# Kernel tuning notes

Measured on AMD Instinct MI355X. Metric: run time of the kernel, lower is better.

## Reference

```python
import jax, jax.numpy as jnp
import numpy as np
from jax import lax

B, T, IN, H, OUT = 64, 2048, 128, 256, 1


def setup_inputs() -> dict:
    key = jax.random.key(0)
    ks = jax.random.split(key, 11)
    s_in = 1.0 / np.sqrt(H)
    return {
        "x": jax.random.normal(ks[0], (B, T, IN), dtype=jnp.float32),
        "W_ih0": jax.random.normal(ks[1], (H, IN), dtype=jnp.float32) * s_in,
        "W_hh0": jax.random.normal(ks[2], (H, H), dtype=jnp.float32) * s_in,
        "b_ih0": jax.random.normal(ks[3], (H,), dtype=jnp.float32) * s_in,
        "b_hh0": jax.random.normal(ks[4], (H,), dtype=jnp.float32) * s_in,
        "W_ih1": jax.random.normal(ks[5], (H, H), dtype=jnp.float32) * s_in,
        "W_hh1": jax.random.normal(ks[6], (H, H), dtype=jnp.float32) * s_in,
        "b_ih1": jax.random.normal(ks[7], (H,), dtype=jnp.float32) * s_in,
        "b_hh1": jax.random.normal(ks[8], (H,), dtype=jnp.float32) * s_in,
        "W_fc": jax.random.normal(ks[9], (OUT, H), dtype=jnp.float32) * s_in,
        "b_fc": jax.random.normal(ks[10], (OUT,), dtype=jnp.float32) * s_in,
    }


def _rnn_layer(inp, W_ih, W_hh, b_ih, b_hh):
    # Precompute input projection for all timesteps in one big GEMM: [B,T,H]
    xp = jnp.einsum('bti,hi->bth', inp, W_ih) + b_ih + b_hh
    h0 = jnp.zeros((inp.shape[0], W_hh.shape[0]), dtype=inp.dtype)

    def step(h, xt):  # xt: [B,H]
        h_new = jnp.tanh(xt + h @ W_hh.T)
        return h_new, h_new

    _, hs = lax.scan(step, h0, jnp.swapaxes(xp, 0, 1))  # hs: [T,B,H]
    return jnp.swapaxes(hs, 0, 1)  # [B,T,H]


def reference(x, W_ih0, W_hh0, b_ih0, b_hh0, W_ih1, W_hh1, b_ih1, b_hh1, W_fc, b_fc):
    h1 = _rnn_layer(x, W_ih0, W_hh0, b_ih0, b_hh0)   # layer 0 (dropout_prob=0.0)
    h2 = _rnn_layer(h1, W_ih1, W_hh1, b_ih1, b_hh1)  # layer 1
    last = h2[:, -1, :]                              # [B,H]
    return last @ W_fc.T + b_fc                      # [B,OUT]
```

## Files before the change

### kernel.cpp

```cpp
#include <hip/hip_runtime.h>
#include <math.h>

constexpr int Bb  = 64;
constexpr int Tt  = 2048;
constexpr int INN = 128;
constexpr int HH  = 256;
constexpr int ROWS = Bb * Tt;
constexpr int CH  = 64;
constexpr int NCH = Tt / CH;
constexpr int PS  = HH + 4;

__device__ int g_flag0[Bb];
__device__ int g_flag1[Bb];

__global__ __launch_bounds__(256) void ih_gemm(const float* in, const float* W,
                                               const float* bias1, const float* bias2,
                                               float* out)
{
    __shared__ float a_lds[16][68];
    __shared__ float b_lds[16][264];

    const int tid = threadIdx.x;
    if (blockIdx.x == 0 && tid < Bb) { g_flag0[tid] = 0; g_flag1[tid] = 0; }

    const int tx  = tid & 31;
    const int ty  = tid >> 5;
    const int row0 = blockIdx.x * 64;

    float acc[8][8];
#pragma unroll
    for (int r = 0; r < 8; ++r)
#pragma unroll
        for (int c = 0; c < 8; ++c) acc[r][c] = 0.f;

    for (int k0 = 0; k0 < INN; k0 += 16) {
#pragma unroll
        for (int i = 0; i < 4; ++i) {
            int e = i * 256 + tid;
            int r = e >> 4, kk = e & 15;
            a_lds[kk][r] = in[(row0 + r) * INN + k0 + kk];
        }
#pragma unroll
        for (int i = 0; i < 16; ++i) {
            int e = i * 256 + tid;
            int j = e >> 4, kk = e & 15;
            b_lds[kk][j] = W[j * INN + k0 + kk];
        }
        __syncthreads();

#pragma unroll
        for (int kk = 0; kk < 16; ++kk) {
            float4 a0 = *(const float4*)&a_lds[kk][ty * 8];
            float4 a1 = *(const float4*)&a_lds[kk][ty * 8 + 4];
            float4 b0 = *(const float4*)&b_lds[kk][tx * 8];
            float4 b1 = *(const float4*)&b_lds[kk][tx * 8 + 4];
            float av[8] = {a0.x, a0.y, a0.z, a0.w, a1.x, a1.y, a1.z, a1.w};
            float bv[8] = {b0.x, b0.y, b0.z, b0.w, b1.x, b1.y, b1.z, b1.w};
#pragma unroll
            for (int r = 0; r < 8; ++r)
#pragma unroll
                for (int c = 0; c < 8; ++c)
                    acc[r][c] += av[r] * bv[c];
        }
        __syncthreads();
    }

    float bsum[8];
#pragma unroll
    for (int c = 0; c < 8; ++c) {
        int j = tx * 8 + c;
        bsum[c] = bias1[j] + bias2[j];
    }
#pragma unroll
    for (int r = 0; r < 8; ++r) {
        int row = row0 + ty * 8 + r;
        float4 o0 = make_float4(acc[r][0] + bsum[0], acc[r][1] + bsum[1],
                                acc[r][2] + bsum[2], acc[r][3] + bsum[3]);
        float4 o1 = make_float4(acc[r][4] + bsum[4], acc[r][5] + bsum[5],
                                acc[r][6] + bsum[6], acc[r][7] + bsum[7]);
        *(float4*)&out[row * HH + tx * 8]     = o0;
        *(float4*)&out[row * HH + tx * 8 + 4] = o1;
    }
}

__device__ __forceinline__ float fast_tanh(float x)
{
    float e = __builtin_amdgcn_exp2f(x * 2.8853900817779268f);
    return fmaf(-2.0f, __builtin_amdgcn_rcpf(e + 1.0f), 1.0f);
}

__device__ __forceinline__ float fold16(float s)
{
    int v = __builtin_amdgcn_ds_swizzle(__float_as_int(s), 0x401F);
    return s + __int_as_float(v);
}

__device__ __forceinline__ float fold32(float s)
{
#if __has_builtin(__builtin_amdgcn_permlane32_swap)
    typedef unsigned uint2v __attribute__((ext_vector_type(2)));
    uint2v r = __builtin_amdgcn_permlane32_swap(__float_as_uint(s), __float_as_uint(s),
                                                false, false);
    return __uint_as_float(r[0]) + __uint_as_float(r[1]);
#else
    return s + __shfl_xor(s, 32, 64);
#endif
}

__device__ __forceinline__ void rnn_step(const float* rd, float* wr,
                                         float*& pw, const float* pr,
                                         float& xg, const float (&wreg)[4][16],
                                         bool lane_lt16)
{
    float xg2 = *pr;

    float s0 = rd[0 * PS], s1 = rd[1 * PS], s2 = rd[2 * PS], s3 = rd[3 * PS];
    float s = (s0 + s1) + (s2 + s3);
    s = fold16(s);
    s = fold32(s);

    float hv = fast_tanh(s + xg);
    if (lane_lt16) *pw = hv;

    float p0 = 0.f, p1 = 0.f, p2 = 0.f, p3 = 0.f;
#pragma unroll
    for (int c = 0; c < 16; ++c) {
        float hcv = __int_as_float(__builtin_amdgcn_readlane(__float_as_int(hv), c));
        p0 = fmaf(wreg[0][c], hcv, p0);
        p1 = fmaf(wreg[1][c], hcv, p1);
        p2 = fmaf(wreg[2][c], hcv, p2);
        p3 = fmaf(wreg[3][c], hcv, p3);
    }
    *(float4*)wr = make_float4(p0, p1, p2, p3);

    __syncthreads();
    xg = xg2;
    pw += HH;
}

template <bool PROD>
__device__ void rnn_role(float* xpb, const float* Whh, float* sh, int b)
{
    float* pbufA = sh;
    float* pbufB = sh + 16 * PS;

    const int tid = threadIdx.x;
    const int w   = tid >> 6;
    const int l   = tid & 63;
    const int g   = l >> 4;
    const int jr  = 16 * w + (l & 15);
    const bool lane_lt16 = (l < 16);

    float wreg[4][16];
#pragma unroll
    for (int r = 0; r < 4; ++r) {
        const float4* wp = (const float4*)&Whh[(size_t)(4 * l + r) * HH + 16 * w];
#pragma unroll
        for (int q = 0; q < 4; ++q) {
            float4 v = wp[q];
            wreg[r][4 * q + 0] = v.x;
            wreg[r][4 * q + 1] = v.y;
            wreg[r][4 * q + 2] = v.z;
            wreg[r][4 * q + 3] = v.w;
        }
    }

    const float* rdA = &pbufA[4 * g * PS + jr];
    const float* rdB = &pbufB[4 * g * PS + jr];
    float*       wrA = &pbufA[w * PS + 4 * l];
    float*       wrB = &pbufB[w * PS + 4 * l];

    *(float4*)wrA = make_float4(0.f, 0.f, 0.f, 0.f);
    float xg = PROD ? xpb[jr] : 0.f;
    float* pw = xpb + jr;
    const float* pr = xpb + HH + jr;
    __syncthreads();

#pragma unroll 1
    for (int c = 0; c < NCH; ++c) {
        if (!PROD) {
            while (__hip_atomic_load(&g_flag1[b], __ATOMIC_ACQUIRE,
                                     __HIP_MEMORY_SCOPE_AGENT) < (c + 1) * CH)
                __builtin_amdgcn_s_sleep(16);
            xg = xpb[(size_t)c * CH * HH + jr];
        }
        const int npairs = (c == NCH - 1) ? (CH / 2 - 1) : (CH / 2);
#pragma unroll 1
        for (int p = 0; p < npairs; ++p) {
            rnn_step(rdA, wrB, pw, pr, xg, wreg, lane_lt16); pr += HH;
            rnn_step(rdB, wrA, pw, pr, xg, wreg, lane_lt16); pr += HH;
        }
        if (c == NCH - 1) {
            rnn_step(rdA, wrB, pw, pr, xg, wreg, lane_lt16);
            rnn_step(rdB, wrA, pw, pr, xg, wreg, lane_lt16);
        }
        if (PROD && tid == 0) {
            __threadfence();
            __hip_atomic_store(&g_flag0[b], (c + 1) * CH,
                               __ATOMIC_RELEASE, __HIP_MEMORY_SCOPE_AGENT);
        }
    }
}

__device__ void gemm_role(float* ws, const float* W,
                          const float* b1, const float* b2, float* sh, int b)
{
    float (*a_lds)[68]  = (float(*)[68])sh;
    float (*b_lds)[264] = (float(*)[264])(sh + 16 * 68);

    const int tid = threadIdx.x;
    const int tx  = tid & 63;
    const int ty  = tid >> 6;

    float bs[4];
#pragma unroll
    for (int q = 0; q < 4; ++q) {
        int j = tx * 4 + q;
        bs[q] = b1[j] + b2[j];
    }

#pragma unroll 1
    for (int c = 0; c < NCH; ++c) {
        while (__hip_atomic_load(&g_flag0[b], __ATOMIC_ACQUIRE,
                                 __HIP_MEMORY_SCOPE_AGENT) < (c + 1) * CH)
            __builtin_amdgcn_s_sleep(16);

        const size_t row0 = (size_t)b * Tt + (size_t)c * CH;
        float acc[4][4];
#pragma unroll
        for (int r = 0; r < 4; ++r)
#pragma unroll
            for (int q = 0; q < 4; ++q) acc[r][q] = 0.f;

        for (int k0 = 0; k0 < HH; k0 += 16) {
            {
                int r = tid >> 4, kk = tid & 15;
                a_lds[kk][r] = ws[(row0 + r) * HH + k0 + kk];
            }
#pragma unroll
            for (int i = 0; i < 4; ++i) {
                int e = i * 1024 + tid;
                int j = e >> 4, kk = e & 15;
                b_lds[kk][j] = W[j * HH + k0 + kk];
            }
            __syncthreads();
#pragma unroll
            for (int kk = 0; kk < 16; ++kk) {
                float4 av = *(const float4*)&a_lds[kk][ty * 4];
                float4 bv = *(const float4*)&b_lds[kk][tx * 4];
                float avs[4] = {av.x, av.y, av.z, av.w};
                float bvs[4] = {bv.x, bv.y, bv.z, bv.w};
#pragma unroll
                for (int r = 0; r < 4; ++r)
#pragma unroll
                    for (int q = 0; q < 4; ++q)
                        acc[r][q] = fmaf(avs[r], bvs[q], acc[r][q]);
            }
            __syncthreads();
        }

#pragma unroll
        for (int r = 0; r < 4; ++r) {
            size_t row = row0 + ty * 4 + r;
            *(float4*)&ws[row * HH + tx * 4] =
                make_float4(acc[r][0] + bs[0], acc[r][1] + bs[1],
                            acc[r][2] + bs[2], acc[r][3] + bs[3]);
        }
        __syncthreads();
        if (tid == 0) {
            __threadfence();
            __hip_atomic_store(&g_flag1[b], (c + 1) * CH,
                               __ATOMIC_RELEASE, __HIP_MEMORY_SCOPE_AGENT);
        }
    }
}

__global__ __launch_bounds__(1024, 4) void pipeline_kernel(
        float* ws, const float* Whh0, const float* Wih1,
        const float* bih1, const float* bhh1, const float* Whh1)
{
    __shared__ __attribute__((aligned(16))) float sh[2 * 16 * PS];

    const int role = blockIdx.x >> 6;
    const int b    = blockIdx.x & 63;

    if (role == 0)
        rnn_role<true>(ws + (size_t)b * Tt * HH, Whh0, sh, b);
    else if (role == 1)
        gemm_role(ws, Wih1, bih1, bhh1, sh, b);
    else
        rnn_role<false>(ws + (size_t)b * Tt * HH, Whh1, sh, b);
}

__global__ __launch_bounds__(64) void fc_kernel(const float* h2, const float* Wfc,
                                                const float* bfc, float* out)
{
    const int b = blockIdx.x;
    const int l = threadIdx.x;
    const float* hrow = h2 + ((size_t)b * Tt + (Tt - 1)) * HH;
    float4 hv = *(const float4*)&hrow[4 * l];
    float4 wv = *(const float4*)&Wfc[4 * l];
    float p = hv.x * wv.x + hv.y * wv.y + hv.z * wv.z + hv.w * wv.w;
#pragma unroll
    for (int off = 32; off > 0; off >>= 1) p += __shfl_down(p, off, 64);
    if (l == 0) out[b] = p + bfc[0];
}

extern "C" void kernel_launch(void* const* d_in, const int* in_sizes, int n_in,
                              void* d_out, int out_size, void* d_ws, size_t ws_size,
                              hipStream_t stream)
{
    const float* x     = (const float*)d_in[0];
    const float* W_ih0 = (const float*)d_in[1];
    const float* W_hh0 = (const float*)d_in[2];
    const float* b_ih0 = (const float*)d_in[3];
    const float* b_hh0 = (const float*)d_in[4];
    const float* W_ih1 = (const float*)d_in[5];
    const float* W_hh1 = (const float*)d_in[6];
    const float* b_ih1 = (const float*)d_in[7];
    const float* b_hh1 = (const float*)d_in[8];
    const float* W_fc  = (const float*)d_in[9];
    const float* b_fc  = (const float*)d_in[10];
    float* ws  = (float*)d_ws;
    float* out = (float*)d_out;

    ih_gemm<<<ROWS / 64, 256, 0, stream>>>(x, W_ih0, b_ih0, b_hh0, ws);
    pipeline_kernel<<<192, 1024, 0, stream>>>(ws, W_hh0, W_ih1, b_ih1, b_hh1, W_hh1);
    fc_kernel<<<Bb, 64, 0, stream>>>(ws, W_fc, b_fc, out);
}
```

Baseline: 1.744 ms.

## Double-buffer layer-1 input GEMM with 8x8 register tiles on 256 compute threads

Reworks the gemm_role that computes the layer-1 input projection for each chunk. It double-buffers the LDS tiles so the next K-slice loads while the current one is computed, cutting one barrier per slice. Only the first 256 threads now compute, each holding an 8x8 accumulator tile, while all 1024 threads share the staging loads. The LDS row padding shrinks from 264 to 260, and the shared array is resized to fit both buffers. The cost is more registers per compute thread and idle compute lanes, which may slow the RNN roles that share this kernel.

Measured after the change: 4.196 ms. 141% more time.

```diff
diff --git a/kernel.cpp b/kernel.cpp
--- a/kernel.cpp
+++ b/kernel.cpp
@@ -18,7 +18,7 @@
                                                float* out)
 {
     __shared__ float a_lds[16][68];
-    __shared__ float b_lds[16][264];
+    __shared__ float b_lds[16][260];
 
     const int tid = threadIdx.x;
     if (blockIdx.x == 0 && tid < Bb) { g_flag0[tid] = 0; g_flag1[tid] = 0; }
@@ -168,13 +168,15 @@
     const float* rdA = &pbufA[4 * g * PS + jr];
     const float* rdB = &pbufB[4 * g * PS + jr];
     float*       wrA = &pbufA[w * PS + 4 * l];
-    float*       wrB = &pbufB[w * PS + 4 * l];
 
     *(float4*)wrA = make_float4(0.f, 0.f, 0.f, 0.f);
     float xg = PROD ? xpb[jr] : 0.f;
     float* pw = xpb + jr;
     const float* pr = xpb + HH + jr;
     __syncthreads();
+
+    float* wrAx = &pbufA[w * PS + 4 * l];
+    float* wrBx = &pbufB[w * PS + 4 * l];
 
 #pragma unroll 1
     for (int c = 0; c < NCH; ++c) {
@@ -187,12 +189,12 @@
         const int npairs = (c == NCH - 1) ? (CH / 2 - 1) : (CH / 2);
 #pragma unroll 1
         for (int p = 0; p < npairs; ++p) {
-            rnn_step(rdA, wrB, pw, pr, xg, wreg, lane_lt16); pr += HH;
-            rnn_step(rdB, wrA, pw, pr, xg, wreg, lane_lt16); pr += HH;
+            rnn_step(rdA, wrBx, pw, pr, xg, wreg, lane_lt16); pr += HH;
+            rnn_step(rdB, wrAx, pw, pr, xg, wreg, lane_lt16); pr += HH;
         }
         if (c == NCH - 1) {
-            rnn_step(rdA, wrB, pw, pr, xg, wreg, lane_lt16);
-            rnn_step(rdB, wrA, pw, pr, xg, wreg, lane_lt16);
+            rnn_step(rdA, wrBx, pw, pr, xg, wreg, lane_lt16);
+            rnn_step(rdB, wrAx, pw, pr, xg, wreg, lane_lt16);
         }
         if (PROD && tid == 0) {
             __threadfence();
@@ -202,22 +204,27 @@
     }
 }
 
+constexpr int ASZ = 16 * 68;
+constexpr int BSZ = 16 * 260;
+
 __device__ void gemm_role(float* ws, const float* W,
                           const float* b1, const float* b2, float* sh, int b)
 {
-    float (*a_lds)[68]  = (float(*)[68])sh;
-    float (*b_lds)[264] = (float(*)[264])(sh + 16 * 68);
-
-    const int tid = threadIdx.x;
-    const int tx  = tid & 63;
-    const int ty  = tid >> 6;
-
-    float bs[4];
-#pragma unroll
-    for (int q = 0; q < 4; ++q) {
-        int j = tx * 4 + q;
-        bs[q] = b1[j] + b2[j];
-    }
+    float* Ad = sh;
+    float* Bd = sh + 2 * ASZ;
+
+    const int tid  = threadIdx.x;
+    const bool comp = (tid < 256);
+    const int tx = tid & 31;
+    const int ty = (tid >> 5) & 7;
+
+    float bs[8];
+    if (comp) {
+#pragma unroll
+        for (int q = 0; q < 8; ++q) bs[q] = b1[tx * 8 + q] + b2[tx * 8 + q];
+    }
+
+    const int sr = tid >> 4, sk = tid & 15;
 
 #pragma unroll 1
     for (int c = 0; c < NCH; ++c) {
@@ -225,48 +232,70 @@
                                  __HIP_MEMORY_SCOPE_AGENT) < (c + 1) * CH)
             __builtin_amdgcn_s_sleep(16);
 
-        const size_t row0 = (size_t)b * Tt + (size_t)c * CH;
-        float acc[4][4];
-#pragma unroll
-        for (int r = 0; r < 4; ++r)
-#pragma unroll
-            for (int q = 0; q < 4; ++q) acc[r][q] = 0.f;
-
-        for (int k0 = 0; k0 < HH; k0 += 16) {
-            {
-                int r = tid >> 4, kk = tid & 15;
-                a_lds[kk][r] = ws[(row0 + r) * HH + k0 + kk];
+        float* Ab = ws + ((size_t)b * Tt + (size_t)c * CH) * HH;
+
+        Ad[sk * 68 + sr] = Ab[(size_t)sr * HH + sk];
+#pragma unroll
+        for (int i = 0; i < 4; ++i) {
+            int e = i * 1024 + tid;
+            int j = e >> 4, k2 = e & 15;
+            Bd[k2 * 260 + j] = W[j * HH + k2];
+        }
+        __syncthreads();
+
+        float acc[8][8];
+        if (comp) {
+#pragma unroll
+            for (int r = 0; r < 8; ++r)
+#pragma unroll
+                for (int q = 0; q < 8; ++q) acc[r][q] = 0.f;
+        }
+
+#pragma unroll 1
+        for (int s = 0; s < 16; ++s) {
+            const int cur = s & 1;
+            if (s < 15) {
+                const int k0 = (s + 1) * 16;
+                Ad[(cur ^ 1) * ASZ + sk * 68 + sr] = Ab[(size_t)sr * HH + k0 + sk];
+#pragma unroll
+                for (int i = 0; i < 4; ++i) {
+                    int e = i * 1024 + tid;
+                    int j = e >> 4, k2 = e & 15;
+                    Bd[(cur ^ 1) * BSZ + k2 * 260 + j] = W[j * HH + k0 + k2];
+                }
             }
-#pragma unroll
-            for (int i = 0; i < 4; ++i) {
-                int e = i * 1024 + tid;
-                int j = e >> 4, kk = e & 15;
-                b_lds[kk][j] = W[j * HH + k0 + kk];
+            if (comp) {
+                const float* Ac = Ad + cur * ASZ;
+                const float* Bc = Bd + cur * BSZ;
+#pragma unroll
+                for (int kk = 0; kk < 16; ++kk) {
+                    float4 a0 = *(const float4*)&Ac[kk * 68 + ty * 8];
+                    float4 a1 = *(const float4*)&Ac[kk * 68 + ty * 8 + 4];
+                    float4 c0 = *(const float4*)&Bc[kk * 260 + tx * 8];
+                    float4 c1 = *(const float4*)&Bc[kk * 260 + tx * 8 + 4];
+                    float av[8] = {a0.x, a0.y, a0.z, a0.w, a1.x, a1.y, a1.z, a1.w};
+                    float bv[8] = {c0.x, c0.y, c0.z, c0.w, c1.x, c1.y, c1.z, c1.w};
+#pragma unroll
+                    for (int r = 0; r < 8; ++r)
+#pragma unroll
+                        for (int q = 0; q < 8; ++q)
+                            acc[r][q] = fmaf(av[r], bv[q], acc[r][q]);
+                }
+                if (s == 15) {
+#pragma unroll
+                    for (int r = 0; r < 8; ++r) {
+                        float* orow = Ab + (size_t)(ty * 8 + r) * HH + tx * 8;
+                        *(float4*)orow =
+                            make_float4(acc[r][0] + bs[0], acc[r][1] + bs[1],
+                                        acc[r][2] + bs[2], acc[r][3] + bs[3]);
+                        *(float4*)(orow + 4) =
+                            make_float4(acc[r][4] + bs[4], acc[r][5] + bs[5],
+                                        acc[r][6] + bs[6], acc[r][7] + bs[7]);
+                    }
+                }
             }
             __syncthreads();
-#pragma unroll
-            for (int kk = 0; kk < 16; ++kk) {
-                float4 av = *(const float4*)&a_lds[kk][ty * 4];
-                float4 bv = *(const float4*)&b_lds[kk][tx * 4];
-                float avs[4] = {av.x, av.y, av.z, av.w};
-                float bvs[4] = {bv.x, bv.y, bv.z, bv.w};
-#pragma unroll
-                for (int r = 0; r < 4; ++r)
-#pragma unroll
-                    for (int q = 0; q < 4; ++q)
-                        acc[r][q] = fmaf(avs[r], bvs[q], acc[r][q]);
-            }
-            __syncthreads();
-        }
-
-#pragma unroll
-        for (int r = 0; r < 4; ++r) {
-            size_t row = row0 + ty * 4 + r;
-            *(float4*)&ws[row * HH + tx * 4] =
-                make_float4(acc[r][0] + bs[0], acc[r][1] + bs[1],
-                            acc[r][2] + bs[2], acc[r][3] + bs[3]);
-        }
-        __syncthreads();
+        }
         if (tid == 0) {
             __threadfence();
             __hip_atomic_store(&g_flag1[b], (c + 1) * CH,
@@ -279,7 +308,7 @@
         float* ws, const float* Whh0, const float* Wih1,
         const float* bih1, const float* bhh1, const float* Whh1)
 {
-    __shared__ __attribute__((aligned(16))) float sh[2 * 16 * PS];
+    __shared__ __attribute__((aligned(16))) float sh[2 * ASZ + 2 * BSZ];
 
     const int role = blockIdx.x >> 6;
     const int b    = blockIdx.x & 63;
```

## Replace per-chunk LDS-tiled GEMM role with register-resident W row-by-row matvec

Applied to the files above, without the earlier changes.

The middle-stage GEMM role (layer-1 input projection per batch chunk) no longer reloads W_ih1 tiles from global into LDS for every 64-row chunk. It now keeps W in registers, loaded once, and computes each row as a matvec using the same readlane/partial-sum/fold scheme as the recurrent role, double-buffering partials in LDS and writing results in place. This removes repeated global weight traffic and LDS tiling overhead, at the cost of one barrier per row and serialized row processing. The ih_gemm b_lds padding also changes from 264 to 260.

New measurement: 2.161 ms. +23.9%, slower.

```diff
diff --git a/kernel.cpp b/kernel.cpp
--- a/kernel.cpp
+++ b/kernel.cpp
@@ -18,7 +18,7 @@
                                                float* out)
 {
     __shared__ float a_lds[16][68];
-    __shared__ float b_lds[16][264];
+    __shared__ float b_lds[16][260];
 
     const int tid = threadIdx.x;
     if (blockIdx.x == 0 && tid < Bb) { g_flag0[tid] = 0; g_flag1[tid] = 0; }
@@ -107,6 +107,38 @@
 #endif
 }
 
+__device__ __forceinline__ void load_wreg(const float* W, int l, int w,
+                                          float (&wreg)[4][16])
+{
+#pragma unroll
+    for (int r = 0; r < 4; ++r) {
+        const float4* wp = (const float4*)&W[(size_t)(4 * l + r) * HH + 16 * w];
+#pragma unroll
+        for (int q = 0; q < 4; ++q) {
+            float4 v = wp[q];
+            wreg[r][4 * q + 0] = v.x;
+            wreg[r][4 * q + 1] = v.y;
+            wreg[r][4 * q + 2] = v.z;
+            wreg[r][4 * q + 3] = v.w;
+        }
+    }
+}
+
+__device__ __forceinline__ void mac_partials(float xg, const float (&wreg)[4][16],
+                                             float* wr)
+{
+    float p0 = 0.f, p1 = 0.f, p2 = 0.f, p3 = 0.f;
+#pragma unroll
+    for (int c = 0; c < 16; ++c) {
+        float hcv = __int_as_float(__builtin_amdgcn_readlane(__float_as_int(xg), c));
+        p0 = fmaf(wreg[0][c], hcv, p0);
+        p1 = fmaf(wreg[1][c], hcv, p1);
+        p2 = fmaf(wreg[2][c], hcv, p2);
+        p3 = fmaf(wreg[3][c], hcv, p3);
+    }
+    *(float4*)wr = make_float4(p0, p1, p2, p3);
+}
+
 __device__ __forceinline__ void rnn_step(const float* rd, float* wr,
                                          float*& pw, const float* pr,
                                          float& xg, const float (&wreg)[4][16],
@@ -122,16 +154,7 @@
     float hv = fast_tanh(s + xg);
     if (lane_lt16) *pw = hv;
 
-    float p0 = 0.f, p1 = 0.f, p2 = 0.f, p3 = 0.f;
-#pragma unroll
-    for (int c = 0; c < 16; ++c) {
-        float hcv = __int_as_float(__builtin_amdgcn_readlane(__float_as_int(hv), c));
-        p0 = fmaf(wreg[0][c], hcv, p0);
-        p1 = fmaf(wreg[1][c], hcv, p1);
-        p2 = fmaf(wreg[2][c], hcv, p2);
-        p3 = fmaf(wreg[3][c], hcv, p3);
-    }
-    *(float4*)wr = make_float4(p0, p1, p2, p3);
+    mac_partials(hv, wreg, wr);
 
     __syncthreads();
     xg = xg2;
@@ -152,18 +175,7 @@
     const bool lane_lt16 = (l < 16);
 
     float wreg[4][16];
-#pragma unroll
-    for (int r = 0; r < 4; ++r) {
-        const float4* wp = (const float4*)&Whh[(size_t)(4 * l + r) * HH + 16 * w];
-#pragma unroll
-        for (int q = 0; q < 4; ++q) {
-            float4 v = wp[q];
-            wreg[r][4 * q + 0] = v.x;
-            wreg[r][4 * q + 1] = v.y;
-            wreg[r][4 * q + 2] = v.z;
-            wreg[r][4 * q + 3] = v.w;
-        }
-    }
+    load_wreg(Whh, l, w, wreg);
 
     const float* rdA = &pbufA[4 * g * PS + jr];
     const float* rdB = &pbufB[4 * g * PS + jr];
@@ -202,22 +214,47 @@
     }
 }
 
+__device__ __forceinline__ void gemm_phase(const float* rd, float* wr,
+                                           float*& pw, const float* pr,
+                                           float& xg, const float (&wreg)[4][16],
+                                           float bsc, bool lane_lt16)
+{
+    float xg2 = *pr;
+
+    float s0 = rd[0 * PS], s1 = rd[1 * PS], s2 = rd[2 * PS], s3 = rd[3 * PS];
+    float s = (s0 + s1) + (s2 + s3);
+    s = fold16(s);
+    s = fold32(s);
+    if (lane_lt16) *pw = s + bsc;
+
+    mac_partials(xg, wreg, wr);
+
+    __syncthreads();
+    xg = xg2;
+    pw += HH;
+}
+
 __device__ void gemm_role(float* ws, const float* W,
                           const float* b1, const float* b2, float* sh, int b)
 {
-    float (*a_lds)[68]  = (float(*)[68])sh;
-    float (*b_lds)[264] = (float(*)[264])(sh + 16 * 68);
+    float* pbufA = sh;
+    float* pbufB = sh + 16 * PS;
 
     const int tid = threadIdx.x;
-    const int tx  = tid & 63;
-    const int ty  = tid >> 6;
-
-    float bs[4];
-#pragma unroll
-    for (int q = 0; q < 4; ++q) {
-        int j = tx * 4 + q;
-        bs[q] = b1[j] + b2[j];
-    }
+    const int w   = tid >> 6;
+    const int l   = tid & 63;
+    const int g   = l >> 4;
+    const int jr  = 16 * w + (l & 15);
+    const bool lane_lt16 = (l < 16);
+
+    float wreg[4][16];
+    load_wreg(W, l, w, wreg);
+    const float bsc = b1[jr] + b2[jr];
+
+    const float* rdA = &pbufA[4 * g * PS + jr];
+    const float* rdB = &pbufB[4 * g * PS + jr];
+    float*       wrA = &pbufA[w * PS + 4 * l];
+    float*       wrB = &pbufB[w * PS + 4 * l];
 
 #pragma unroll 1
     for (int c = 0; c < NCH; ++c) {
@@ -225,48 +262,34 @@
                                  __HIP_MEMORY_SCOPE_AGENT) < (c + 1) * CH)
             __builtin_amdgcn_s_sleep(16);
 
-        const size_t row0 = (size_t)b * Tt + (size_t)c * CH;
-        float acc[4][4];
-#pragma unroll
-        for (int r = 0; r < 4; ++r)
-#pragma unroll
-            for (int q = 0; q < 4; ++q) acc[r][q] = 0.f;
-
-        for (int k0 = 0; k0 < HH; k0 += 16) {
-            {
-                int r = tid >> 4, kk = tid & 15;
-                a_lds[kk][r] = ws[(row0 + r) * HH + k0 + kk];
-            }
-#pragma unroll
-            for (int i = 0; i < 4; ++i) {
-                int e = i * 1024 + tid;
-                int j = e >> 4, kk = e & 15;
-                b_lds[kk][j] = W[j * HH + k0 + kk];
-            }
+        float* Ab = ws + ((size_t)b * Tt + (size_t)c * CH) * HH;
+
+        float xg  = Ab[jr];
+        float xg2 = Ab[HH + jr];
+        mac_partials(xg, wreg, wrB);
+        __syncthreads();
+        xg = xg2;
+
+        float* pw = Ab + jr;
+        const float* pr = Ab + 2 * HH + jr;
+
+#pragma unroll 1
+        for (int p = 0; p < 31; ++p) {
+            gemm_phase(rdB, wrA, pw, pr, xg, wreg, bsc, lane_lt16); pr += HH;
+            gemm_phase(rdA, wrB, pw, pr, xg, wreg, bsc, lane_lt16); pr += HH;
+        }
+        gemm_phase(rdB, wrA, pw, pr - HH, xg, wreg, bsc, lane_lt16);
+
+        {
+            float s0 = rdA[0 * PS], s1 = rdA[1 * PS];
+            float s2 = rdA[2 * PS], s3 = rdA[3 * PS];
+            float s = (s0 + s1) + (s2 + s3);
+            s = fold16(s);
+            s = fold32(s);
+            if (lane_lt16) *pw = s + bsc;
             __syncthreads();
-#pragma unroll
-            for (int kk = 0; kk < 16; ++kk) {
-                float4 av = *(const float4*)&a_lds[kk][ty * 4];
-                float4 bv = *(const float4*)&b_lds[kk][tx * 4];
-                float avs[4] = {av.x, av.y, av.z, av.w};
-                float bvs[4] = {bv.x, bv.y, bv.z, bv.w};
-#pragma unroll
-                for (int r = 0; r < 4; ++r)
-#pragma unroll
-                    for (int q = 0; q < 4; ++q)
-                        acc[r][q] = fmaf(avs[r], bvs[q], acc[r][q]);
-            }
-            __syncthreads();
-        }
-
-#pragma unroll
-        for (int r = 0; r < 4; ++r) {
-            size_t row = row0 + ty * 4 + r;
-            *(float4*)&ws[row * HH + tx * 4] =
-                make_float4(acc[r][0] + bs[0], acc[r][1] + bs[1],
-                            acc[r][2] + bs[2], acc[r][3] + bs[3]);
-        }
-        __syncthreads();
+        }
+
         if (tid == 0) {
             __threadfence();
             __hip_atomic_store(&g_flag1[b], (c + 1) * CH,
```
